# Optimization experiments

Measured on AMD Instinct MI355X. Metric: run time of the kernel, lower is better.

## Reference

```python
import jax, jax.numpy as jnp
import numpy as np

B, N, D_MODEL, H = 4, 4096, 1024, 16
DEPTH = D_MODEL // H
EPS_Z = 1e-9
EPS_LN = 1e-6


def setup_inputs() -> dict:
    key = jax.random.key(0)
    ks = jax.random.split(key, 12)
    s = 1.0 / np.sqrt(D_MODEL)
    return {
        "query": jax.random.normal(ks[0], (B, N, D_MODEL), jnp.float32),
        "key": jax.random.normal(ks[1], (B, N, D_MODEL), jnp.float32),
        "value": jax.random.normal(ks[2], (B, N, D_MODEL), jnp.float32),
        "Wq": jax.random.normal(ks[3], (D_MODEL, D_MODEL), jnp.float32) * s,
        "bq": jnp.zeros((D_MODEL,), jnp.float32),
        "Wk": jax.random.normal(ks[4], (D_MODEL, D_MODEL), jnp.float32) * s,
        "bk": jnp.zeros((D_MODEL,), jnp.float32),
        "Wv": jax.random.normal(ks[5], (D_MODEL, D_MODEL), jnp.float32) * s,
        "bv": jnp.zeros((D_MODEL,), jnp.float32),
        "Wo": jax.random.normal(ks[6], (D_MODEL, D_MODEL), jnp.float32) * s,
        "bo": jnp.zeros((D_MODEL,), jnp.float32),
        "gamma": jnp.ones((D_MODEL,), jnp.float32),
        "beta": jnp.zeros((D_MODEL,), jnp.float32),
    }


def _split_heads(x):
    # [B, N, d_model] -> [B, H, N, depth]
    b, n, _ = x.shape
    return x.reshape(b, n, H, DEPTH).transpose(0, 2, 1, 3)


def reference(query, key, value, Wq, bq, Wk, bk, Wv, bv, Wo, bo, gamma, beta):
    Q = _split_heads(query @ Wq + bq)
    K = _split_heads(key @ Wk + bk)
    V = _split_heads(value @ Wv + bv)

    Q = jax.nn.elu(Q) + 1.0
    K = jax.nn.elu(K) + 1.0

    # Normalizer: Z[b,h,n] = K[b,h,n,:] . sum_l Q[b,h,l,:]
    q_sum = jnp.sum(Q, axis=2)                          # [B,H,d]
    Z = jnp.einsum('bhnd,bhd->bhn', K, q_sum)[..., None]  # [B,H,N,1]

    # output[b,h,m,e] = sum_l sum_d K[l,d] V[m,d] Q[l,e]
    #                 = sum_d V[m,d] * (sum_l K[l,d] Q[l,e])
    KtQ = jnp.einsum('bhld,bhle->bhde', K, Q)           # [B,H,d,d]
    out = jnp.einsum('bhmd,bhde->bhme', V, KtQ)         # [B,H,N,d]
    out = out / (Z + EPS_Z)

    # combine heads -> [B, N, d_model]
    out = out.transpose(0, 2, 1, 3).reshape(query.shape[0], -1, D_MODEL)
    attn = out @ Wo + bo

    x = query + attn
    mu = jnp.mean(x, axis=-1, keepdims=True)
    var = jnp.mean(jnp.square(x - mu), axis=-1, keepdims=True)
    return (x - mu) * jax.lax.rsqrt(var + EPS_LN) * gamma + beta
```

## Files before the change

### kernel.cpp

```cpp
#include <hip/hip_runtime.h>
#include <hip/hip_bf16.h>


typedef __attribute__((ext_vector_type(8))) short short8;
typedef __attribute__((ext_vector_type(4))) float floatx4;
typedef __attribute__((ext_vector_type(4))) unsigned short ushortx4;
typedef __attribute__((ext_vector_type(8))) unsigned short ushortx8;

#define DEVINL __device__ __forceinline__

DEVINL unsigned short f2bf(float f) {
  unsigned int u = __builtin_bit_cast(unsigned int, f);
  u += 0x7fffu + ((u >> 16) & 1u);
  return (unsigned short)(u >> 16);
}
DEVINL float bf2f(unsigned short h) {
  unsigned int u = ((unsigned int)h) << 16;
  return __builtin_bit_cast(float, u);
}
DEVINL void g2l16(const void* g, void* l) {
  __builtin_amdgcn_global_load_lds((const __attribute__((address_space(1))) void*)g,
                                   (__attribute__((address_space(3))) void*)l, 16, 0, 0);
}

__global__ __launch_bounds__(256) void conv_kernel(const float* __restrict__ in,
                                                   unsigned short* __restrict__ out) {
  const size_t i = ((size_t)blockIdx.x * 256 + threadIdx.x) * 8;
  const float4 a = *(const float4*)(in + i);
  const float4 b = *(const float4*)(in + i + 4);
  ushortx8 o;
  o[0] = f2bf(a.x); o[1] = f2bf(a.y); o[2] = f2bf(a.z); o[3] = f2bf(a.w);
  o[4] = f2bf(b.x); o[5] = f2bf(b.y); o[6] = f2bf(b.z); o[7] = f2bf(b.w);
  *(ushortx8*)(out + i) = o;
}

struct W4 { const float* w[4]; };

__global__ __launch_bounds__(256) void wtrans_kernel(W4 wp, unsigned short* wt) {
  const int z = blockIdx.z;
  const float* W = wp.w[z];
  unsigned short* WT = wt + (size_t)z * 1024 * 1024;
  __shared__ float tile[32][33];
  const int bx = blockIdx.x, by = blockIdx.y;
  const int t = threadIdx.x, r = t >> 5, c = t & 31;
#pragma unroll
  for (int p = 0; p < 4; ++p)
    tile[p * 8 + r][c] = W[(size_t)(by * 32 + p * 8 + r) * 1024 + bx * 32 + c];
  __syncthreads();
#pragma unroll
  for (int p = 0; p < 4; ++p)
    WT[(size_t)(bx * 32 + p * 8 + r) * 1024 + by * 32 + c] = f2bf(tile[c][p * 8 + r]);
}

__global__ __launch_bounds__(512, 2) void gemm_bt_kernel(const unsigned short* __restrict__ A,
                                                         const unsigned short* __restrict__ BT,
                                                         const float* __restrict__ bias,
                                                         unsigned short* __restrict__ C,
                                                         int act, int qsflag, int zflag,
                                                         float* qsum, float* Z,
                                                         int M, int N, int K) {
  const int mb = M >> 8;
  const int id = blockIdx.x;
  const int m0 = (id % mb) << 8;
  const int n0 = (id / mb) << 8;
  __shared__ unsigned short smem[65536];
  const int t = threadIdx.x, lane = t & 63, wave = t >> 6;
  const int wm = wave >> 2, wn = wave & 3;
  const int srow = lane >> 3;
  const int scol = ((lane & 7) ^ srow) * 8;
  const int rl = lane & 15, qw = lane >> 4;
  const int NT = K >> 6;

  floatx4 acc[8][4] = {};

  const unsigned short* Ag = A + (size_t)m0 * K;
  const unsigned short* Bg = BT + (size_t)n0 * K;

#define LA(c) (smem + (c) * 32768)
#define LB(c) (smem + (c) * 32768 + 16384)

  auto STG = [&](unsigned short* Lt, const unsigned short* Gt, int R, int k0) {
    const int r0 = R + wave * 8;
    g2l16(Gt + (size_t)(r0 + srow) * K + (k0 + scol), (void*)(Lt + r0 * 64));
  };

  STG(LB(0), Bg, 0, 0);    STG(LB(0), Bg, 64, 0);
  STG(LB(0), Bg, 128, 0);  STG(LB(0), Bg, 192, 0);
  STG(LA(0), Ag, 0, 0);    STG(LA(0), Ag, 128, 0);
  STG(LA(0), Ag, 64, 0);   STG(LA(0), Ag, 192, 0);
  STG(LB(1), Bg, 0, 64);   STG(LB(1), Bg, 64, 64);
  STG(LB(1), Bg, 128, 64); STG(LB(1), Bg, 192, 64);
  STG(LA(1), Ag, 0, 64);   STG(LA(1), Ag, 128, 64);
  asm volatile("s_waitcnt vmcnt(6)" ::: "memory");
  __builtin_amdgcn_s_barrier();

  for (int tk = 0; tk < NT; ++tk) {
    unsigned short* lAc = LA(tk & 1);
    unsigned short* lBc = LB(tk & 1);
    short8 bf[4][2];
#pragma unroll
    for (int q = 0; q < 4; ++q) {
      if (q == 0) {
#pragma unroll
        for (int nt = 0; nt < 4; ++nt)
#pragma unroll
          for (int ks = 0; ks < 2; ++ks)
            bf[nt][ks] = *(const short8*)&lBc[(wn * 64 + nt * 16 + rl) * 64 +
                                              (((ks * 4 + qw) ^ (rl & 7)) * 8)];
      }
      short8 af[2][2];
#pragma unroll
      for (int mt = 0; mt < 2; ++mt)
#pragma unroll
        for (int ks = 0; ks < 2; ++ks)
          af[mt][ks] = *(const short8*)&lAc[(wm * 128 + q * 32 + mt * 16 + rl) * 64 +
                                            (((ks * 4 + qw) ^ (rl & 7)) * 8)];
      if (q == 0) {
        if (tk + 1 < NT) {
          const int k1 = (tk + 1) << 6;
          unsigned short* lAn = LA((tk + 1) & 1);
          STG(lAn, Ag, 64, k1); STG(lAn, Ag, 192, k1);
        }
      } else if (q == 1) {
        if (tk + 2 < NT) { const int k2 = (tk + 2) << 6; STG(lBc, Bg, 0, k2); STG(lBc, Bg, 64, k2); }
      } else if (q == 2) {
        if (tk + 2 < NT) { const int k2 = (tk + 2) << 6; STG(lBc, Bg, 128, k2); STG(lBc, Bg, 192, k2); }
      } else {
        if (tk + 2 < NT) { const int k2 = (tk + 2) << 6; STG(lAc, Ag, 0, k2); STG(lAc, Ag, 128, k2); }
      }
      __builtin_amdgcn_s_barrier();
      asm volatile("s_waitcnt lgkmcnt(0)" ::: "memory");
      __builtin_amdgcn_s_setprio(1);
#pragma unroll
      for (int ks = 0; ks < 2; ++ks)
#pragma unroll
        for (int mt = 0; mt < 2; ++mt)
#pragma unroll
          for (int nt = 0; nt < 4; ++nt)
            acc[q * 2 + mt][nt] = __builtin_amdgcn_mfma_f32_16x16x32_bf16(
                af[mt][ks], bf[nt][ks], acc[q * 2 + mt][nt], 0, 0, 0);
      __builtin_amdgcn_s_setprio(0);
      if (q == 3 && tk + 1 < NT) {
        if (tk + 1 == NT - 1) asm volatile("s_waitcnt vmcnt(0)" ::: "memory");
        else                  asm volatile("s_waitcnt vmcnt(6)" ::: "memory");
      }
      __builtin_amdgcn_s_barrier();
    }
  }

  __syncthreads();
  const int bb = m0 >> 12;
  float cs[4] = {0.f, 0.f, 0.f, 0.f};
  float zacc[8][4];
#pragma unroll
  for (int mt = 0; mt < 8; ++mt)
#pragma unroll
    for (int r = 0; r < 4; ++r) zacc[mt][r] = 0.f;

#pragma unroll
  for (int nt = 0; nt < 4; ++nt) {
    const int coll = wn * 64 + nt * 16 + rl;
    const int colg = n0 + coll;
    const float bv = bias[colg];
    float qsv = 0.f;
    if (zflag) qsv = qsum[(bb * 16 + (colg >> 6)) * 64 + (colg & 63)];
    const int chnk = wn * 4 + nt;
#pragma unroll
    for (int mt = 0; mt < 8; ++mt) {
#pragma unroll
      for (int r = 0; r < 4; ++r) {
        const int rowl = wm * 128 + mt * 16 + qw * 4 + r;
        float v = acc[mt][nt][r] + bv;
        if (act) v = (v > 0.f) ? (v + 1.f) : __expf(v);
        cs[nt] += v;
        if (zflag) zacc[mt][r] += v * qsv;
        smem[rowl * 256 + ((chnk ^ (rowl & 15)) * 16) + rl] = f2bf(v);
      }
    }
  }
  __syncthreads();
#pragma unroll
  for (int i = 0; i < 16; ++i) {
    const int idx = i * 512 + t;
    const int row = idx >> 5;
    const int seg = idx & 31;
    const int phys = (seg >> 1) ^ (row & 15);
    *(short8*)(C + (size_t)(m0 + row) * N + n0 + seg * 8) =
        *(const short8*)&smem[row * 256 + phys * 16 + (seg & 1) * 8];
  }

  if (qsflag) {
#pragma unroll
    for (int nt = 0; nt < 4; ++nt) {
      float v = cs[nt];
      v += __shfl_xor(v, 16);
      v += __shfl_xor(v, 32);
      if (lane < 16) {
        const int colg = n0 + wn * 64 + nt * 16 + lane;
        atomicAdd(&qsum[(bb * 16 + (colg >> 6)) * 64 + (colg & 63)], v);
      }
    }
  }
  if (zflag) {
    const int h = (n0 >> 6) + wn;
#pragma unroll
    for (int mt = 0; mt < 8; ++mt) {
#pragma unroll
      for (int r = 0; r < 4; ++r) {
        float v = zacc[mt][r];
        v += __shfl_xor(v, 1); v += __shfl_xor(v, 2);
        v += __shfl_xor(v, 4); v += __shfl_xor(v, 8);
        if ((lane & 15) == 0) {
          const int rowg = m0 + wm * 128 + mt * 16 + qw * 4 + r;
          Z[((size_t)(bb * 16 + h)) * 4096 + (rowg & 4095)] = v;
        }
      }
    }
  }
}

#define KTS 136
__global__ __launch_bounds__(256) void ktq_partial_kernel(const unsigned short* Qp,
                                                          const unsigned short* Kp,
                                                          float* part) {
  const int bh = blockIdx.x, b = bh >> 4, h = bh & 15;
  const int s = blockIdx.y;
  const unsigned short* Qh = Qp + (size_t)b * 4096 * 1024 + h * 64;
  const unsigned short* Kh = Kp + (size_t)b * 4096 * 1024 + h * 64;
  __shared__ unsigned short Kt[64 * KTS];
  __shared__ unsigned short Qt[64 * KTS];
  const int t = threadIdx.x, lane = t & 63, wave = t >> 6;
  floatx4 acc[4] = {};
  const int nlb = t >> 3;
  const int dblk = (t & 7) * 8;

  for (int c0 = s * 512; c0 < s * 512 + 512; c0 += 128) {
    __syncthreads();
#pragma unroll
    for (int it = 0; it < 4; ++it) {
      const int nl = it * 32 + nlb;
      const size_t goff = (size_t)(c0 + nl) * 1024 + dblk;
      short8 kv = *(const short8*)(Kh + goff);
      short8 qv = *(const short8*)(Qh + goff);
#pragma unroll
      for (int j = 0; j < 8; ++j) {
        Kt[(dblk + j) * KTS + nl] = (unsigned short)kv[j];
        Qt[(dblk + j) * KTS + nl] = (unsigned short)qv[j];
      }
    }
    __syncthreads();
#pragma unroll
    for (int ks = 0; ks < 4; ++ks) {
      const short8 a = *(const short8*)&Kt[(wave * 16 + (lane & 15)) * KTS + ks * 32 + (lane >> 4) * 8];
#pragma unroll
      for (int et = 0; et < 4; ++et) {
        const short8 bb = *(const short8*)&Qt[(et * 16 + (lane & 15)) * KTS + ks * 32 + (lane >> 4) * 8];
        acc[et] = __builtin_amdgcn_mfma_f32_16x16x32_bf16(a, bb, acc[et], 0, 0, 0);
      }
    }
  }
  float* outp = part + ((size_t)(s * 64 + bh)) * 4096;
#pragma unroll
  for (int et = 0; et < 4; ++et) {
    const int e = et * 16 + (lane & 15);
#pragma unroll
    for (int r = 0; r < 4; ++r) {
      const int d = wave * 16 + (lane >> 4) * 4 + r;
      outp[e * 64 + d] = acc[et][r];
    }
  }
}

__global__ __launch_bounds__(256) void ktq_reduce_kernel(const float* __restrict__ part,
                                                         unsigned short* __restrict__ ktqt) {
  const int bh = blockIdx.x, t = threadIdx.x;
#pragma unroll
  for (int i = 0; i < 16; ++i) {
    const int idx = i * 256 + t;
    float s = 0.f;
#pragma unroll
    for (int sl = 0; sl < 8; ++sl) s += part[((size_t)(sl * 64 + bh)) * 4096 + idx];
    ktqt[(size_t)bh * 4096 + idx] = f2bf(s);
  }
}

#define CTS 72
__global__ __launch_bounds__(256) void stagec_kernel(const unsigned short* Vp,
                                                     const unsigned short* ktqt,
                                                     const float* __restrict__ Z,
                                                     unsigned short* U) {
  const int bh = blockIdx.y, b = bh >> 4, h = bh & 15;
  const int n0 = blockIdx.x * 256;
  __shared__ unsigned short kt_lds[64 * CTS];
  __shared__ float zbuf[256];
  const int t = threadIdx.x, lane = t & 63, wave = t >> 6;

  {
    const unsigned short* src = ktqt + (size_t)bh * 4096;
    const int row = t >> 2, seg = (t & 3) * 16;
    *(short8*)&kt_lds[row * CTS + seg] = *(const short8*)(src + row * 64 + seg);
    *(short8*)&kt_lds[row * CTS + seg + 8] = *(const short8*)(src + row * 64 + seg + 8);
  }
  zbuf[t] = Z[(size_t)bh * 4096 + n0 + t];
  __syncthreads();

  const unsigned short* Vh = Vp + (size_t)b * 4096 * 1024 + h * 64;
  floatx4 acc[4][4] = {};
#pragma unroll
  for (int ks = 0; ks < 2; ++ks) {
    short8 bfr[4];
#pragma unroll
    for (int et = 0; et < 4; ++et)
      bfr[et] = *(const short8*)&kt_lds[(et * 16 + (lane & 15)) * CTS + ks * 32 + (lane >> 4) * 8];
#pragma unroll
    for (int mt = 0; mt < 4; ++mt) {
      const short8 a = *(const short8*)(Vh + (size_t)(n0 + wave * 64 + mt * 16 + (lane & 15)) * 1024 +
                                        ks * 32 + (lane >> 4) * 8);
#pragma unroll
      for (int et = 0; et < 4; ++et)
        acc[mt][et] = __builtin_amdgcn_mfma_f32_16x16x32_bf16(a, bfr[et], acc[mt][et], 0, 0, 0);
    }
  }
#pragma unroll
  for (int mt = 0; mt < 4; ++mt) {
#pragma unroll
    for (int r = 0; r < 4; ++r) {
      const int rl = wave * 64 + mt * 16 + (lane >> 4) * 4 + r;
      const float inv = 1.0f / (zbuf[rl] + 1e-9f);
#pragma unroll
      for (int et = 0; et < 4; ++et) {
        const int e = et * 16 + (lane & 15);
        U[((size_t)b * 4096 + n0 + rl) * 1024 + h * 64 + e] = f2bf(acc[mt][et][r] * inv);
      }
    }
  }
}

__global__ __launch_bounds__(256) void ln_kernel(const float* query, const unsigned short* attn,
                                                 const float* gamma, const float* beta, float* out) {
  const int row = blockIdx.x, t = threadIdx.x;
  const float* qrow = query + (size_t)row * 1024;
  const unsigned short* arow = attn + (size_t)row * 1024;
  const float4 qv = *(const float4*)(qrow + t * 4);
  const ushortx4 av = *(const ushortx4*)(arow + t * 4);
  float x0 = qv.x + bf2f(av.x), x1 = qv.y + bf2f(av.y);
  float x2 = qv.z + bf2f(av.z), x3 = qv.w + bf2f(av.w);
  float s = x0 + x1 + x2 + x3;
  float s2 = x0 * x0 + x1 * x1 + x2 * x2 + x3 * x3;
  for (int off = 32; off > 0; off >>= 1) {
    s += __shfl_down(s, off);
    s2 += __shfl_down(s2, off);
  }
  __shared__ float lred[8];
  if ((t & 63) == 0) { lred[(t >> 6) * 2] = s; lred[(t >> 6) * 2 + 1] = s2; }
  __syncthreads();
  s = lred[0] + lred[2] + lred[4] + lred[6];
  s2 = lred[1] + lred[3] + lred[5] + lred[7];
  const float mu = s * (1.f / 1024.f);
  const float var = s2 * (1.f / 1024.f) - mu * mu;
  const float rstd = rsqrtf(var + 1e-6f);
  float4 o;
  o.x = (x0 - mu) * rstd * gamma[t * 4 + 0] + beta[t * 4 + 0];
  o.y = (x1 - mu) * rstd * gamma[t * 4 + 1] + beta[t * 4 + 1];
  o.z = (x2 - mu) * rstd * gamma[t * 4 + 2] + beta[t * 4 + 2];
  o.w = (x3 - mu) * rstd * gamma[t * 4 + 3] + beta[t * 4 + 3];
  *(float4*)(out + (size_t)row * 1024 + t * 4) = o;
}

extern "C" void kernel_launch(void* const* d_in, const int* in_sizes, int n_in,
                              void* d_out, int out_size, void* d_ws, size_t ws_size,
                              hipStream_t stream) {
  const float* query = (const float*)d_in[0];
  const float* key_  = (const float*)d_in[1];
  const float* value = (const float*)d_in[2];
  const float* Wq = (const float*)d_in[3];
  const float* bq = (const float*)d_in[4];
  const float* Wk = (const float*)d_in[5];
  const float* bk = (const float*)d_in[6];
  const float* Wv = (const float*)d_in[7];
  const float* bv = (const float*)d_in[8];
  const float* Wo = (const float*)d_in[9];
  const float* bo = (const float*)d_in[10];
  const float* gamma = (const float*)d_in[11];
  const float* beta = (const float*)d_in[12];
  float* out = (float*)d_out;

  char* ws = (char*)d_ws;
  unsigned short* abf = (unsigned short*)(ws + 0);
  unsigned short* Qp = (unsigned short*)(ws + 33554432);
  unsigned short* Kp = (unsigned short*)(ws + 67108864);
  unsigned short* Vp = (unsigned short*)(ws + 100663296);
  unsigned short* WT = (unsigned short*)(ws + 134217728);
  float* qsumP = (float*)(ws + 142606336);
  unsigned short* ktqtP = (unsigned short*)(ws + 142606336 + 16384);
  float* Zp = (float*)(ws + 142606336 + 16384 + 524288);
  float* part = (float*)abf;
  unsigned short* U = abf;
  unsigned short* attn = Qp;

  dim3 blk(256);
  dim3 gblk(512);

  W4 w4; w4.w[0] = Wq; w4.w[1] = Wk; w4.w[2] = Wv; w4.w[3] = Wo;
  wtrans_kernel<<<dim3(32, 32, 4), blk, 0, stream>>>(w4, WT);

  hipMemsetAsync(qsumP, 0, 64 * 64 * sizeof(float), stream);

  const int convGrid = 8192;
  const int gemmGrid = 64 * 4;

  conv_kernel<<<convGrid, blk, 0, stream>>>(query, abf);
  gemm_bt_kernel<<<gemmGrid, gblk, 0, stream>>>(abf, WT, bq, Qp, 1, 1, 0, qsumP, Zp,
                                                16384, 1024, 1024);

  conv_kernel<<<convGrid, blk, 0, stream>>>(key_, abf);
  gemm_bt_kernel<<<gemmGrid, gblk, 0, stream>>>(abf, WT + 1024 * 1024, bk, Kp, 1, 0, 1,
                                                qsumP, Zp, 16384, 1024, 1024);

  conv_kernel<<<convGrid, blk, 0, stream>>>(value, abf);
  gemm_bt_kernel<<<gemmGrid, gblk, 0, stream>>>(abf, WT + 2 * 1024 * 1024, bv, Vp, 0, 0, 0,
                                                qsumP, Zp, 16384, 1024, 1024);

  ktq_partial_kernel<<<dim3(64, 8), blk, 0, stream>>>(Qp, Kp, part);
  ktq_reduce_kernel<<<64, blk, 0, stream>>>(part, ktqtP);
  stagec_kernel<<<dim3(16, 64), blk, 0, stream>>>(Vp, ktqtP, Zp, U);

  gemm_bt_kernel<<<gemmGrid, gblk, 0, stream>>>(U, WT + 3 * 1024 * 1024, bo, attn, 0, 0, 0,
                                                qsumP, Zp, 16384, 1024, 1024);

  ln_kernel<<<16384, blk, 0, stream>>>(query, attn, gamma, beta, out);
}
```

Measured before the change: 498.1 us.

## Double-buffer LDS fragments in registers to overlap loads with MFMA

Restructures the GEMM main loop so that the A and B fragments for the next quarter-step (and the next K tile) are read from LDS into a second register buffer while the current MFMAs run. The loop is unrolled by two so the buffer index is known at compile time, and partial lgkmcnt waits replace the full drain before each compute phase. Barriers are also reduced and moved. This aims to hide LDS read latency behind matrix work, but it costs more VGPRs, which may reduce occupancy or cause spills. It also assumes NT is even.

```diff
diff --git a/kernel.cpp b/kernel.cpp
--- a/kernel.cpp
+++ b/kernel.cpp
@@ -83,6 +83,9 @@
     const int r0 = R + wave * 8;
     g2l16(Gt + (size_t)(r0 + srow) * K + (k0 + scol), (void*)(Lt + r0 * 64));
   };
+  auto FRAG = [&](const unsigned short* Lt, int row, int ks) -> short8 {
+    return *(const short8*)&Lt[row * 64 + (((ks * 4 + qw) ^ (rl & 7)) * 8)];
+  };
 
   STG(LB(0), Bg, 0, 0);    STG(LB(0), Bg, 64, 0);
   STG(LB(0), Bg, 128, 0);  STG(LB(0), Bg, 192, 0);
@@ -94,57 +97,77 @@
   asm volatile("s_waitcnt vmcnt(6)" ::: "memory");
   __builtin_amdgcn_s_barrier();
 
-  for (int tk = 0; tk < NT; ++tk) {
-    unsigned short* lAc = LA(tk & 1);
-    unsigned short* lBc = LB(tk & 1);
-    short8 bf[4][2];
-#pragma unroll
-    for (int q = 0; q < 4; ++q) {
-      if (q == 0) {
-#pragma unroll
-        for (int nt = 0; nt < 4; ++nt)
-#pragma unroll
-          for (int ks = 0; ks < 2; ++ks)
-            bf[nt][ks] = *(const short8*)&lBc[(wn * 64 + nt * 16 + rl) * 64 +
-                                              (((ks * 4 + qw) ^ (rl & 7)) * 8)];
-      }
-      short8 af[2][2];
-#pragma unroll
-      for (int mt = 0; mt < 2; ++mt)
+  short8 af[2][2][2];
+  short8 bfr[2][4][2];
+#pragma unroll
+  for (int nt = 0; nt < 4; ++nt)
+#pragma unroll
+    for (int ks = 0; ks < 2; ++ks)
+      bfr[0][nt][ks] = FRAG(LB(0), wn * 64 + nt * 16 + rl, ks);
+#pragma unroll
+  for (int mt = 0; mt < 2; ++mt)
+#pragma unroll
+    for (int ks = 0; ks < 2; ++ks)
+      af[0][mt][ks] = FRAG(LA(0), wm * 128 + mt * 16 + rl, ks);
+
+  for (int tt = 0; tt < NT; tt += 2) {
+#pragma unroll
+    for (int h = 0; h < 2; ++h) {
+      const int tk = tt + h;
+      unsigned short* lAc = LA(h);
+      unsigned short* lBc = LB(h);
+      unsigned short* lAn = LA(h ^ 1);
+      unsigned short* lBn = LB(h ^ 1);
+#pragma unroll
+      for (int q = 0; q < 4; ++q) {
+        if (q == 0) {
+          if (tk + 1 < NT) { const int k1 = (tk + 1) << 6; STG(lAn, Ag, 64, k1); STG(lAn, Ag, 192, k1); }
+        } else if (q == 1) {
+          if (tk + 2 < NT) { const int k2 = (tk + 2) << 6; STG(lBc, Bg, 0, k2); STG(lBc, Bg, 64, k2); }
+        } else if (q == 2) {
+          if (tk + 2 < NT) { const int k2 = (tk + 2) << 6; STG(lBc, Bg, 128, k2); STG(lBc, Bg, 192, k2); }
+        } else {
+          if (tk + 2 < NT) { const int k2 = (tk + 2) << 6; STG(lAc, Ag, 0, k2); STG(lAc, Ag, 128, k2); }
+          if (tk + 1 < NT) {
+            if (tk + 1 == NT - 1) asm volatile("s_waitcnt vmcnt(0)" ::: "memory");
+            else                  asm volatile("s_waitcnt vmcnt(6)" ::: "memory");
+          }
+          __builtin_amdgcn_s_barrier();
+        }
+        if (q < 3) {
+#pragma unroll
+          for (int mt = 0; mt < 2; ++mt)
+#pragma unroll
+            for (int ks = 0; ks < 2; ++ks)
+              af[(q + 1) & 1][mt][ks] = FRAG(lAc, wm * 128 + (q + 1) * 32 + mt * 16 + rl, ks);
+          asm volatile("s_waitcnt lgkmcnt(4)" ::: "memory");
+        } else if (tk + 1 < NT) {
+#pragma unroll
+          for (int nt = 0; nt < 4; ++nt)
+#pragma unroll
+            for (int ks = 0; ks < 2; ++ks)
+              bfr[h ^ 1][nt][ks] = FRAG(lBn, wn * 64 + nt * 16 + rl, ks);
+#pragma unroll
+          for (int mt = 0; mt < 2; ++mt)
+#pragma unroll
+            for (int ks = 0; ks < 2; ++ks)
+              af[0][mt][ks] = FRAG(lAn, wm * 128 + mt * 16 + rl, ks);
+          asm volatile("s_waitcnt lgkmcnt(12)" ::: "memory");
+        } else {
+          asm volatile("s_waitcnt lgkmcnt(0)" ::: "memory");
+        }
+        __builtin_amdgcn_s_setprio(1);
 #pragma unroll
         for (int ks = 0; ks < 2; ++ks)
-          af[mt][ks] = *(const short8*)&lAc[(wm * 128 + q * 32 + mt * 16 + rl) * 64 +
-                                            (((ks * 4 + qw) ^ (rl & 7)) * 8)];
-      if (q == 0) {
-        if (tk + 1 < NT) {
-          const int k1 = (tk + 1) << 6;
-          unsigned short* lAn = LA((tk + 1) & 1);
-          STG(lAn, Ag, 64, k1); STG(lAn, Ag, 192, k1);
-        }
-      } else if (q == 1) {
-        if (tk + 2 < NT) { const int k2 = (tk + 2) << 6; STG(lBc, Bg, 0, k2); STG(lBc, Bg, 64, k2); }
-      } else if (q == 2) {
-        if (tk + 2 < NT) { const int k2 = (tk + 2) << 6; STG(lBc, Bg, 128, k2); STG(lBc, Bg, 192, k2); }
-      } else {
-        if (tk + 2 < NT) { const int k2 = (tk + 2) << 6; STG(lAc, Ag, 0, k2); STG(lAc, Ag, 128, k2); }
-      }
-      __builtin_amdgcn_s_barrier();
-      asm volatile("s_waitcnt lgkmcnt(0)" ::: "memory");
-      __builtin_amdgcn_s_setprio(1);
-#pragma unroll
-      for (int ks = 0; ks < 2; ++ks)
-#pragma unroll
-        for (int mt = 0; mt < 2; ++mt)
-#pragma unroll
-          for (int nt = 0; nt < 4; ++nt)
-            acc[q * 2 + mt][nt] = __builtin_amdgcn_mfma_f32_16x16x32_bf16(
-                af[mt][ks], bf[nt][ks], acc[q * 2 + mt][nt], 0, 0, 0);
-      __builtin_amdgcn_s_setprio(0);
-      if (q == 3 && tk + 1 < NT) {
-        if (tk + 1 == NT - 1) asm volatile("s_waitcnt vmcnt(0)" ::: "memory");
-        else                  asm volatile("s_waitcnt vmcnt(6)" ::: "memory");
-      }
-      __builtin_amdgcn_s_barrier();
+#pragma unroll
+          for (int mt = 0; mt < 2; ++mt)
+#pragma unroll
+            for (int nt = 0; nt < 4; ++nt)
+              acc[q * 2 + mt][nt] = __builtin_amdgcn_mfma_f32_16x16x32_bf16(
+                  af[q & 1][mt][ks], bfr[h][nt][ks], acc[q * 2 + mt][nt], 0, 0, 0);
+        __builtin_amdgcn_s_setprio(0);
+        __builtin_amdgcn_s_barrier();
+      }
     }
   }
 
```

After: 663.9 us. 1.33x slower.
